# Optimization experiments

Measured on AMD Instinct MI355X. Metric: run time of the kernel, lower is better.

## Reference

```python
import jax, jax.numpy as jnp
import numpy as np
from jax import lax

N = 64          # n (even -> odd=0, add_odd=0)
B = 256         # batch
F = 256         # input_features
ITERS = 10      # sinkhorn iterations


def _conv1d(x, w, b, pad, dil):
    # x: (B, Cin, L), w: (Cout, Cin, K) torch layout
    y = lax.conv_general_dilated(
        x, w, window_strides=(1,), padding=[(pad, pad)],
        rhs_dilation=(dil,), dimension_numbers=("NCH", "OIH", "NCH"))
    return y + b[None, :, None]


def setup_inputs() -> dict:
    key = jax.random.key(0)
    ks = jax.random.split(key, 17)
    s = 0.02
    d = {
        "x": jax.random.normal(ks[0], (B, F), jnp.float32),
        # linear stack (torch Linear layout: (out, in))
        "w1": jax.random.normal(ks[1], (2 * N, F), jnp.float32) * s,
        "b1": jax.random.normal(ks[2], (2 * N,), jnp.float32) * s,
        "w2": jax.random.normal(ks[3], (N * N, 2 * N), jnp.float32) * s,
        "b2": jax.random.normal(ks[4], (N * N,), jnp.float32) * s,
        "w3": jax.random.normal(ks[5], (4 * N * N, N * N), jnp.float32) * s,
        "b3": jax.random.normal(ks[6], (4 * N * N,), jnp.float32) * s,
        # conv stack: 2n->3n->2n->n->n->n, all k=3
        "cw1": jax.random.normal(ks[7], (3 * N, 2 * N, 3), jnp.float32) * s,
        "cb1": jax.random.normal(ks[8], (3 * N,), jnp.float32) * s,
        "cw2": jax.random.normal(ks[9], (2 * N, 3 * N, 3), jnp.float32) * s,
        "cb2": jax.random.normal(ks[10], (2 * N,), jnp.float32) * s,
        "cw3": jax.random.normal(ks[11], (N, 2 * N, 3), jnp.float32) * s,
        "cb3": jax.random.normal(ks[12], (N,), jnp.float32) * s,
        "cw4": jax.random.normal(ks[13], (N, N, 3), jnp.float32) * s,
        "cb4": jax.random.normal(ks[14], (N,), jnp.float32) * s,
        "cw5": jax.random.normal(ks[15], (N, N, 3), jnp.float32) * s,
        "cb5": jax.random.normal(ks[16], (N,), jnp.float32) * s,
    }
    return d


def _sink(x, iters):
    # output = x + 0.001; repeat: row-normalize then col-normalize
    out = x + 0.001

    def body(o, _):
        o = o / jnp.sum(o, axis=2, keepdims=True)  # row_sink: divide each row by its sum
        o = o / jnp.sum(o, axis=1, keepdims=True)  # col_sink: divide each column by its sum
        return o, None

    out, _ = lax.scan(body, out, None, length=iters)
    return out


def reference(x, w1, b1, w2, b2, w3, b3,
              cw1, cb1, cw2, cb2, cw3, cb3, cw4, cb4, cw5, cb5):
    h = x @ w1.T + b1
    h = h @ w2.T + b2
    h = h @ w3.T + b3                      # (B, 4n^2)
    h = h.reshape(B, 2 * N, 2 * N)         # (B, 128, 128)
    # conv1: p=0, d=(n-8)//2=28 (since n>10); rest pad=0, dil=1
    h = _conv1d(h, cw1, cb1, 0, (N - 8) // 2)  # (B, 192, 72)
    h = _conv1d(h, cw2, cb2, 0, 1)             # (B, 128, 70)
    h = _conv1d(h, cw3, cb3, 0, 1)             # (B, 64, 68)
    h = _conv1d(h, cw4, cb4, 0, 1)             # (B, 64, 66)
    h = _conv1d(h, cw5, cb5, 0, 1)             # (B, 64, 64)
    h = h * h                                   # torch.pow(x, 2)
    return _sink(h, ITERS)
```

## Files before the change

kernel.cpp:

```cpp
#include <hip/hip_runtime.h>
#include <hip/hip_bf16.h>

typedef float f32x4 __attribute__((ext_vector_type(4)));
typedef __bf16 bf16x8 __attribute__((ext_vector_type(8)));

typedef __attribute__((address_space(1))) const unsigned int as1_uint;
typedef __attribute__((address_space(3))) unsigned int as3_uint;

__global__ __launch_bounds__(128) void gemm1_k(const float* __restrict__ x,
                                               const float* __restrict__ w1,
                                               const float* __restrict__ b1,
                                               float* __restrict__ h1) {
    __shared__ float xs[256];
    const int m = blockIdx.x, t = threadIdx.x;
    xs[t] = x[m * 256 + t];
    xs[t + 128] = x[m * 256 + 128 + t];
    __syncthreads();
    float acc = b1[t];
    const float4* wr = (const float4*)(w1 + t * 256);
#pragma unroll 8
    for (int k4 = 0; k4 < 64; ++k4) {
        float4 w = wr[k4];
        acc += xs[k4 * 4 + 0] * w.x + xs[k4 * 4 + 1] * w.y +
               xs[k4 * 4 + 2] * w.z + xs[k4 * 4 + 3] * w.w;
    }
    h1[m * 128 + t] = acc;
}

__global__ __launch_bounds__(256) void gemm2_k(const float* __restrict__ h1,
                                               const float* __restrict__ w2,
                                               const float* __restrict__ b2,
                                               char* __restrict__ h2b) {
    __shared__ float As[64][129];
    __shared__ float Bs[64][129];
    const int nb = blockIdx.x, mb = blockIdx.y, t = threadIdx.x;
#pragma unroll
    for (int i = 0; i < 8; ++i) {
        int idx = i * 256 + t;
        int row = idx >> 5, c4 = (idx & 31) * 4;
        float4 a = *(const float4*)(h1 + (mb * 64 + row) * 128 + c4);
        As[row][c4 + 0] = a.x; As[row][c4 + 1] = a.y;
        As[row][c4 + 2] = a.z; As[row][c4 + 3] = a.w;
        float4 bv = *(const float4*)(w2 + (nb * 64 + row) * 128 + c4);
        Bs[row][c4 + 0] = bv.x; Bs[row][c4 + 1] = bv.y;
        Bs[row][c4 + 2] = bv.z; Bs[row][c4 + 3] = bv.w;
    }
    __syncthreads();
    const int tx = t & 15, ty = t >> 4;
    float acc[4][4] = {};
#pragma unroll 4
    for (int k = 0; k < 128; ++k) {
        float a[4], b[4];
#pragma unroll
        for (int i = 0; i < 4; ++i) a[i] = As[ty * 4 + i][k];
#pragma unroll
        for (int j = 0; j < 4; ++j) b[j] = Bs[tx * 4 + j][k];
#pragma unroll
        for (int i = 0; i < 4; ++i)
#pragma unroll
            for (int j = 0; j < 4; ++j) acc[i][j] += a[i] * b[j];
    }
#pragma unroll
    for (int i = 0; i < 4; ++i)
#pragma unroll
        for (int j = 0; j < 4; ++j) {
            int m = mb * 64 + ty * 4 + i;
            int n = nb * 64 + tx * 4 + j;
            float v = acc[i][j] + b2[n];
            int kb = n >> 6, r = n & 63;
            int byte = kb * 32768 + ((m * 128 + (r >> 3) * 16) ^ ((m & 7) << 4)) + (r & 7) * 2;
            *(__bf16*)(h2b + byte) = (__bf16)v;
        }
}

__global__ __launch_bounds__(512, 1) void gemm3_k(const char* __restrict__ Ab,
                                                  const float* __restrict__ W,
                                                  const float* __restrict__ bias,
                                                  float* __restrict__ C) {
    __shared__ __align__(16) char lds[81920];
    const int tid = threadIdx.x;
    const int n0 = blockIdx.x * 64;
    const int lane = tid & 63, wid = tid >> 6;
    const int mrow = tid >> 3, kb8 = tid & 7;

#define ISSUE_A(t, buf)                                                          \
    {                                                                            \
        const char* _s = Ab + (t) * 32768 + wid * 4096 + lane * 16;              \
        char* _d = lds + (buf) * 32768 + wid * 4096;                             \
        __builtin_amdgcn_global_load_lds((as1_uint*)(_s), (as3_uint*)(_d), 16, 0, 0);          \
        __builtin_amdgcn_global_load_lds((as1_uint*)(_s + 1024), (as3_uint*)(_d + 1024), 16, 0, 0); \
        __builtin_amdgcn_global_load_lds((as1_uint*)(_s + 2048), (as3_uint*)(_d + 2048), 16, 0, 0); \
        __builtin_amdgcn_global_load_lds((as1_uint*)(_s + 3072), (as3_uint*)(_d + 3072), 16, 0, 0); \
    }

    float4 w0, w1;
    auto loadW = [&](int t) {
        const float* q = W + (n0 + mrow) * 4096 + t * 64 + kb8 * 8;
        w0 = *(const float4*)q;
        w1 = *(const float4*)(q + 4);
    };
    auto storeW = [&](int buf) {
        bf16x8 p;
        p[0] = (__bf16)w0.x; p[1] = (__bf16)w0.y; p[2] = (__bf16)w0.z; p[3] = (__bf16)w0.w;
        p[4] = (__bf16)w1.x; p[5] = (__bf16)w1.y; p[6] = (__bf16)w1.z; p[7] = (__bf16)w1.w;
        *(bf16x8*)(lds + 65536 + buf * 8192 +
                   ((mrow * 128 + kb8 * 16) ^ ((mrow & 7) << 4))) = p;
    };

    ISSUE_A(0, 0);
    loadW(0);
    __syncthreads();
    storeW(0);
    __syncthreads();

    const int lr = lane & 15, lq = lane >> 4;
    const int wm = wid >> 1, wn = wid & 1;

    f32x4 acc[4][2];
    const f32x4 zero = {0.f, 0.f, 0.f, 0.f};
#pragma unroll
    for (int mi = 0; mi < 4; ++mi)
#pragma unroll
        for (int ni = 0; ni < 2; ++ni) acc[mi][ni] = zero;

    for (int t = 0; t < 64; ++t) {
        const int cur = t & 1;
        if (t < 63) {
            ISSUE_A(t + 1, cur ^ 1);
            loadW(t + 1);
        }
        const char* Ac = lds + cur * 32768;
        const char* Wc = lds + 65536 + cur * 8192;
#pragma unroll
        for (int kk = 0; kk < 2; ++kk) {
            const int kb = kk * 4 + lq;
            bf16x8 af[4], bfv[2];
#pragma unroll
            for (int mi = 0; mi < 4; ++mi) {
                int m = wm * 64 + mi * 16 + lr;
                af[mi] = *(const bf16x8*)(Ac + ((m * 128 + kb * 16) ^ ((m & 7) << 4)));
            }
#pragma unroll
            for (int ni = 0; ni < 2; ++ni) {
                int n = wn * 32 + ni * 16 + lr;
                bfv[ni] = *(const bf16x8*)(Wc + ((n * 128 + kb * 16) ^ ((n & 7) << 4)));
            }
#pragma unroll
            for (int mi = 0; mi < 4; ++mi)
#pragma unroll
                for (int ni = 0; ni < 2; ++ni)
                    acc[mi][ni] = __builtin_amdgcn_mfma_f32_16x16x32_bf16(
                        af[mi], bfv[ni], acc[mi][ni], 0, 0, 0);
        }
        __syncthreads();
        if (t < 63) storeW(cur ^ 1);
        __syncthreads();
    }
#undef ISSUE_A

    float bv[2];
#pragma unroll
    for (int ni = 0; ni < 2; ++ni) bv[ni] = bias[n0 + wn * 32 + ni * 16 + lr];
#pragma unroll
    for (int mi = 0; mi < 4; ++mi)
#pragma unroll
        for (int ni = 0; ni < 2; ++ni) {
            const int n = n0 + wn * 32 + ni * 16 + lr;
#pragma unroll
            for (int r = 0; r < 4; ++r) {
                int m = wm * 64 + mi * 16 + lq * 4 + r;
                C[m * 16384 + n] = acc[mi][ni][r] + bv[ni];
            }
        }
}

template <int CIN, int COUT, int DIL, int MT, int NT>
__device__ __forceinline__ void conv_core(const char* xt, char* wl,
                                          const float* __restrict__ w,
                                          f32x4 (&acc)[MT][NT], int tid) {
    constexpr int RB = CIN * 2;
    const int lane = tid & 63, wid = tid >> 6;
    const int lr = lane & 15, lq = lane >> 4;
    const int cobase = wid * (COUT / 4);
    const f32x4 zero = {0.f, 0.f, 0.f, 0.f};
#pragma unroll
    for (int mi = 0; mi < MT; ++mi)
#pragma unroll
        for (int ni = 0; ni < NT; ++ni) acc[mi][ni] = zero;

    for (int cic = 0; cic < CIN / 32; ++cic) {
        for (int idx = tid; idx < COUT * 4; idx += 256) {
            int co = idx >> 2, cib = idx & 3, ci0 = cic * 32 + cib * 8;
            const float* src = w + co * (CIN * 3) + ci0 * 3;
            float v[24];
#pragma unroll
            for (int u = 0; u < 6; ++u) {
                float4 f = *(const float4*)(src + u * 4);
                v[u * 4 + 0] = f.x; v[u * 4 + 1] = f.y;
                v[u * 4 + 2] = f.z; v[u * 4 + 3] = f.w;
            }
#pragma unroll
            for (int tp = 0; tp < 3; ++tp) {
                bf16x8 pk;
#pragma unroll
                for (int j = 0; j < 8; ++j) pk[j] = (__bf16)v[j * 3 + tp];
                *(bf16x8*)(wl + ((tp * 4 + cib) * COUT + co) * 16) = pk;
            }
        }
        __syncthreads();
#pragma unroll
        for (int tp = 0; tp < 3; ++tp) {
            bf16x8 af[MT];
#pragma unroll
            for (int mi = 0; mi < MT; ++mi)
                af[mi] = *(const bf16x8*)(wl + ((tp * 4 + lq) * COUT + cobase + mi * 16 + lr) * 16);
            bf16x8 bfr[NT];
#pragma unroll
            for (int ni = 0; ni < NT; ++ni) {
                int colX = ni * 16 + lr + tp * DIL;
                bfr[ni] = *(const bf16x8*)(xt + ((colX * RB + (cic * 4 + lq) * 16) ^ ((colX & 7) << 4)));
            }
#pragma unroll
            for (int mi = 0; mi < MT; ++mi)
#pragma unroll
                for (int ni = 0; ni < NT; ++ni)
                    acc[mi][ni] = __builtin_amdgcn_mfma_f32_16x16x32_bf16(
                        af[mi], bfr[ni], acc[mi][ni], 0, 0, 0);
        }
        __syncthreads();
    }
}

template <int COUT, int LOUT, int MT, int NT>
__device__ __forceinline__ void write_xt(char* xt_out, const f32x4 (&acc)[MT][NT],
                                         const float* __restrict__ bias, int tid) {
    constexpr int RBO = COUT * 2;
    const int lane = tid & 63, wid = tid >> 6;
    const int lr = lane & 15, lq = lane >> 4;
    const int cobase = wid * (COUT / 4);
#pragma unroll
    for (int mi = 0; mi < MT; ++mi)
#pragma unroll
        for (int ni = 0; ni < NT; ++ni) {
            int l = ni * 16 + lr;
            if (l < LOUT) {
#pragma unroll
                for (int r = 0; r < 4; ++r) {
                    int co = cobase + mi * 16 + lq * 4 + r;
                    float y = acc[mi][ni][r] + bias[co];
                    int byte = (l * RBO + ((co >> 3) << 4) + (co & 7) * 2) ^ ((l & 7) << 4);
                    *(__bf16*)(xt_out + byte) = (__bf16)y;
                }
            }
        }
}

__global__ __launch_bounds__(256, 1) void convsink_k(
    const float* __restrict__ h3,
    const float* __restrict__ cw1, const float* __restrict__ cb1,
    const float* __restrict__ cw2, const float* __restrict__ cb2,
    const float* __restrict__ cw3, const float* __restrict__ cb3,
    const float* __restrict__ cw4, const float* __restrict__ cb4,
    const float* __restrict__ cw5, const float* __restrict__ cb5,
    float* __restrict__ out) {
    __shared__ __align__(16) char lds[34816 + 31488 + 36864 + 16640];
    char* xtA = lds;
    char* xtB = lds + 34816;
    char* wl = lds + 34816 + 31488;
    float* S = (float*)(lds + 34816 + 31488 + 36864);

    const int b = blockIdx.x, tid = threadIdx.x;
    const float* src = h3 + b * 16384;

#pragma unroll
    for (int i = 0; i < 8; ++i) {
        int idx = i * 256 + tid;
        int l = idx & 127, cib = idx >> 7;
        bf16x8 p;
#pragma unroll
        for (int j = 0; j < 8; ++j) p[j] = (__bf16)src[(cib * 8 + j) * 128 + l];
        *(bf16x8*)(xtA + ((l * 256 + cib * 16) ^ ((l & 7) << 4))) = p;
    }
    __syncthreads();

    {
        f32x4 acc[3][5];
        conv_core<128, 192, 28, 3, 5>(xtA, wl, cw1, acc, tid);
        write_xt<192, 72, 3, 5>(xtB, acc, cb1, tid);
    }
    __syncthreads();
    {
        f32x4 acc[2][5];
        conv_core<192, 128, 1, 2, 5>(xtB, wl, cw2, acc, tid);
        write_xt<128, 70, 2, 5>(xtA, acc, cb2, tid);
    }
    __syncthreads();
    {
        f32x4 acc[1][5];
        conv_core<128, 64, 1, 1, 5>(xtA, wl, cw3, acc, tid);
        write_xt<64, 68, 1, 5>(xtB, acc, cb3, tid);
    }
    __syncthreads();
    {
        f32x4 acc[1][5];
        conv_core<64, 64, 1, 1, 5>(xtB, wl, cw4, acc, tid);
        write_xt<64, 66, 1, 5>(xtA, acc, cb4, tid);
    }
    __syncthreads();
    {
        f32x4 acc[1][4];
        conv_core<64, 64, 1, 1, 4>(xtA, wl, cw5, acc, tid);
        const int lane = tid & 63, wid = tid >> 6;
        const int lr = lane & 15, lq = lane >> 4;
        const int cobase = wid * 16;
#pragma unroll
        for (int ni = 0; ni < 4; ++ni) {
            int l = ni * 16 + lr;
#pragma unroll
            for (int r = 0; r < 4; ++r) {
                int co = cobase + lq * 4 + r;
                float y = acc[0][ni][r] + cb5[co];
                S[co * 65 + l] = y * y + 0.001f;
            }
        }
    }
    __syncthreads();

    const int q = tid & 3, rid = tid >> 2;
    for (int it = 0; it < 10; ++it) {
        float p = 0.f;
#pragma unroll
        for (int j = 0; j < 16; ++j) p += S[rid * 65 + q * 16 + j];
        p += __shfl_xor(p, 1);
        p += __shfl_xor(p, 2);
        float inv = 1.0f / p;
#pragma unroll
        for (int j = 0; j < 16; ++j) S[rid * 65 + q * 16 + j] *= inv;
        __syncthreads();
        float c = 0.f;
#pragma unroll
        for (int i = 0; i < 16; ++i) c += S[(q * 16 + i) * 65 + rid];
        c += __shfl_xor(c, 1);
        c += __shfl_xor(c, 2);
        float invc = 1.0f / c;
#pragma unroll
        for (int i = 0; i < 16; ++i) S[(q * 16 + i) * 65 + rid] *= invc;
        __syncthreads();
    }

#pragma unroll
    for (int i = 0; i < 16; ++i) {
        int idx = i * 256 + tid;
        out[b * 4096 + idx] = S[(idx >> 6) * 65 + (idx & 63)];
    }
}

extern "C" void kernel_launch(void* const* d_in, const int* in_sizes, int n_in,
                              void* d_out, int out_size, void* d_ws, size_t ws_size,
                              hipStream_t stream) {
    const float* x = (const float*)d_in[0];
    const float* w1 = (const float*)d_in[1];
    const float* b1 = (const float*)d_in[2];
    const float* w2 = (const float*)d_in[3];
    const float* b2 = (const float*)d_in[4];
    const float* w3 = (const float*)d_in[5];
    const float* b3 = (const float*)d_in[6];
    const float* cw1 = (const float*)d_in[7];
    const float* cb1 = (const float*)d_in[8];
    const float* cw2 = (const float*)d_in[9];
    const float* cb2 = (const float*)d_in[10];
    const float* cw3 = (const float*)d_in[11];
    const float* cb3 = (const float*)d_in[12];
    const float* cw4 = (const float*)d_in[13];
    const float* cb4 = (const float*)d_in[14];
    const float* cw5 = (const float*)d_in[15];
    const float* cb5 = (const float*)d_in[16];
    float* out = (float*)d_out;

    char* ws = (char*)d_ws;
    float* h1 = (float*)(ws);
    char* h2b = ws + 131072;
    float* h3 = (float*)(ws + 131072 + 2097152);

    gemm1_k<<<256, 128, 0, stream>>>(x, w1, b1, h1);
    gemm2_k<<<dim3(64, 4), 256, 0, stream>>>(h1, w2, b2, h2b);
    gemm3_k<<<256, 512, 0, stream>>>(h2b, w3, b3, h3);
    convsink_k<<<256, 256, 0, stream>>>(h3, cw1, cb1, cw2, cb2, cw3, cb3,
                                        cw4, cb4, cw5, cb5, out);
}
```

Baseline: 150.1 us.

## Triple-buffer A tiles with two-ahead prefetch and a single barrier per step

Extends the A operand staging in the third GEMM from double to triple LDS buffering, with the async global-to-LDS loads issued two iterations ahead. The two full __syncthreads per iteration become a single s_barrier preceded by a manual lgkmcnt wait. Read completion of the A prefetch relies on the in-order vmcnt wait the compiler inserts for the W register loads. The goal is to hide global load latency and cut synchronization stalls, at the cost of more LDS per block (still one block per CU) and fragile hand-managed wait counts.

```diff
diff --git a/kernel.cpp b/kernel.cpp
--- a/kernel.cpp
+++ b/kernel.cpp
@@ -77,41 +77,45 @@
                                                   const float* __restrict__ W,
                                                   const float* __restrict__ bias,
                                                   float* __restrict__ C) {
-    __shared__ __align__(16) char lds[81920];
+    __shared__ __align__(16) char lds[3 * 32768 + 2 * 8192];
+    char* const Wb = lds + 98304;
     const int tid = threadIdx.x;
     const int n0 = blockIdx.x * 64;
     const int lane = tid & 63, wid = tid >> 6;
     const int mrow = tid >> 3, kb8 = tid & 7;
 
-#define ISSUE_A(t, buf)                                                          \
-    {                                                                            \
-        const char* _s = Ab + (t) * 32768 + wid * 4096 + lane * 16;              \
-        char* _d = lds + (buf) * 32768 + wid * 4096;                             \
-        __builtin_amdgcn_global_load_lds((as1_uint*)(_s), (as3_uint*)(_d), 16, 0, 0);          \
+#define ISSUE_A(t, slot)                                                            \
+    {                                                                               \
+        const char* _s = Ab + (t) * 32768 + wid * 4096 + lane * 16;                 \
+        char* _d = lds + (slot) * 32768 + wid * 4096;                               \
+        __builtin_amdgcn_global_load_lds((as1_uint*)(_s), (as3_uint*)(_d), 16, 0, 0);             \
         __builtin_amdgcn_global_load_lds((as1_uint*)(_s + 1024), (as3_uint*)(_d + 1024), 16, 0, 0); \
         __builtin_amdgcn_global_load_lds((as1_uint*)(_s + 2048), (as3_uint*)(_d + 2048), 16, 0, 0); \
         __builtin_amdgcn_global_load_lds((as1_uint*)(_s + 3072), (as3_uint*)(_d + 3072), 16, 0, 0); \
     }
 
-    float4 w0, w1;
+    float4 w0r, w1r;
     auto loadW = [&](int t) {
         const float* q = W + (n0 + mrow) * 4096 + t * 64 + kb8 * 8;
-        w0 = *(const float4*)q;
-        w1 = *(const float4*)(q + 4);
+        w0r = *(const float4*)q;
+        w1r = *(const float4*)(q + 4);
     };
     auto storeW = [&](int buf) {
         bf16x8 p;
-        p[0] = (__bf16)w0.x; p[1] = (__bf16)w0.y; p[2] = (__bf16)w0.z; p[3] = (__bf16)w0.w;
-        p[4] = (__bf16)w1.x; p[5] = (__bf16)w1.y; p[6] = (__bf16)w1.z; p[7] = (__bf16)w1.w;
-        *(bf16x8*)(lds + 65536 + buf * 8192 +
-                   ((mrow * 128 + kb8 * 16) ^ ((mrow & 7) << 4))) = p;
+        p[0] = (__bf16)w0r.x; p[1] = (__bf16)w0r.y; p[2] = (__bf16)w0r.z; p[3] = (__bf16)w0r.w;
+        p[4] = (__bf16)w1r.x; p[5] = (__bf16)w1r.y; p[6] = (__bf16)w1r.z; p[7] = (__bf16)w1r.w;
+        *(bf16x8*)(Wb + buf * 8192 + ((mrow * 128 + kb8 * 16) ^ ((mrow & 7) << 4))) = p;
     };
 
+    loadW(0);
     ISSUE_A(0, 0);
-    loadW(0);
-    __syncthreads();
+    ISSUE_A(1, 1);
     storeW(0);
-    __syncthreads();
+    asm volatile("s_waitcnt vmcnt(4)" ::: "memory");
+    __builtin_amdgcn_sched_barrier(0);
+    asm volatile("s_waitcnt lgkmcnt(0)" ::: "memory");
+    __builtin_amdgcn_sched_barrier(0);
+    __builtin_amdgcn_s_barrier();
 
     const int lr = lane & 15, lq = lane >> 4;
     const int wm = wid >> 1, wn = wid & 1;
@@ -123,14 +127,15 @@
 #pragma unroll
         for (int ni = 0; ni < 2; ++ni) acc[mi][ni] = zero;
 
+    int sA = 0;
+    int sA2 = 2;
     for (int t = 0; t < 64; ++t) {
         const int cur = t & 1;
-        if (t < 63) {
-            ISSUE_A(t + 1, cur ^ 1);
-            loadW(t + 1);
-        }
-        const char* Ac = lds + cur * 32768;
-        const char* Wc = lds + 65536 + cur * 8192;
+        if (t < 63) loadW(t + 1);
+        if (t < 62) ISSUE_A(t + 2, sA2);
+
+        const char* Ac = lds + sA * 32768;
+        const char* Wc = Wb + cur * 8192;
 #pragma unroll
         for (int kk = 0; kk < 2; ++kk) {
             const int kb = kk * 4 + lq;
@@ -152,9 +157,15 @@
                     acc[mi][ni] = __builtin_amdgcn_mfma_f32_16x16x32_bf16(
                         af[mi], bfv[ni], acc[mi][ni], 0, 0, 0);
         }
-        __syncthreads();
-        if (t < 63) storeW(cur ^ 1);
-        __syncthreads();
+
+        if (t < 63) {
+            storeW(cur ^ 1);
+            asm volatile("s_waitcnt lgkmcnt(0)" ::: "memory");
+            __builtin_amdgcn_sched_barrier(0);
+            __builtin_amdgcn_s_barrier();
+        }
+        sA = (sA == 2) ? 0 : sA + 1;
+        sA2 = (sA2 == 2) ? 0 : sA2 + 1;
     }
 #undef ISSUE_A
 
```

After: 144.2 us. 1.04x faster.

## Drop LDS staging in gemm3 and load MFMA fragments directly from global

Applied to the files above, without the earlier changes.

Rewrites gemm3 so each wave loads its A (bf16) and W (fp32, converted in registers) MFMA fragments straight from global memory into registers, double-buffered across k-steps, with no LDS and no block barriers. gemm2 now writes h2 in an unswizzled layout to match. This removes the LDS round trip and the syncthreads pairs per iteration. In exchange, A and W fragments are reloaded redundantly by several waves, so L2/global traffic rises, and register pressure goes up. The final loop iteration also issues a redundant load of tile 62.

```diff
diff --git a/kernel.cpp b/kernel.cpp
--- a/kernel.cpp
+++ b/kernel.cpp
@@ -3,9 +3,6 @@
 
 typedef float f32x4 __attribute__((ext_vector_type(4)));
 typedef __bf16 bf16x8 __attribute__((ext_vector_type(8)));
-
-typedef __attribute__((address_space(1))) const unsigned int as1_uint;
-typedef __attribute__((address_space(3))) unsigned int as3_uint;
 
 __global__ __launch_bounds__(128) void gemm1_k(const float* __restrict__ x,
                                                const float* __restrict__ w1,
@@ -68,54 +65,63 @@
             int n = nb * 64 + tx * 4 + j;
             float v = acc[i][j] + b2[n];
             int kb = n >> 6, r = n & 63;
-            int byte = kb * 32768 + ((m * 128 + (r >> 3) * 16) ^ ((m & 7) << 4)) + (r & 7) * 2;
+            int byte = kb * 32768 + m * 128 + (r >> 3) * 16 + (r & 7) * 2;
             *(__bf16*)(h2b + byte) = (__bf16)v;
         }
 }
 
-__global__ __launch_bounds__(512, 1) void gemm3_k(const char* __restrict__ Ab,
-                                                  const float* __restrict__ W,
-                                                  const float* __restrict__ bias,
-                                                  float* __restrict__ C) {
-    __shared__ __align__(16) char lds[81920];
+__device__ __forceinline__ bf16x8 pack8(const float4& lo, const float4& hi) {
+    bf16x8 p;
+    p[0] = (__bf16)lo.x; p[1] = (__bf16)lo.y; p[2] = (__bf16)lo.z; p[3] = (__bf16)lo.w;
+    p[4] = (__bf16)hi.x; p[5] = (__bf16)hi.y; p[6] = (__bf16)hi.z; p[7] = (__bf16)hi.w;
+    return p;
+}
+
+__global__ __launch_bounds__(512) void gemm3_k(const char* __restrict__ Ab,
+                                               const float* __restrict__ W,
+                                               const float* __restrict__ bias,
+                                               float* __restrict__ C) {
     const int tid = threadIdx.x;
     const int n0 = blockIdx.x * 64;
     const int lane = tid & 63, wid = tid >> 6;
-    const int mrow = tid >> 3, kb8 = tid & 7;
-
-#define ISSUE_A(t, buf)                                                          \
-    {                                                                            \
-        const char* _s = Ab + (t) * 32768 + wid * 4096 + lane * 16;              \
-        char* _d = lds + (buf) * 32768 + wid * 4096;                             \
-        __builtin_amdgcn_global_load_lds((as1_uint*)(_s), (as3_uint*)(_d), 16, 0, 0);          \
-        __builtin_amdgcn_global_load_lds((as1_uint*)(_s + 1024), (as3_uint*)(_d + 1024), 16, 0, 0); \
-        __builtin_amdgcn_global_load_lds((as1_uint*)(_s + 2048), (as3_uint*)(_d + 2048), 16, 0, 0); \
-        __builtin_amdgcn_global_load_lds((as1_uint*)(_s + 3072), (as3_uint*)(_d + 3072), 16, 0, 0); \
-    }
-
-    float4 w0, w1;
-    auto loadW = [&](int t) {
-        const float* q = W + (n0 + mrow) * 4096 + t * 64 + kb8 * 8;
-        w0 = *(const float4*)q;
-        w1 = *(const float4*)(q + 4);
-    };
-    auto storeW = [&](int buf) {
-        bf16x8 p;
-        p[0] = (__bf16)w0.x; p[1] = (__bf16)w0.y; p[2] = (__bf16)w0.z; p[3] = (__bf16)w0.w;
-        p[4] = (__bf16)w1.x; p[5] = (__bf16)w1.y; p[6] = (__bf16)w1.z; p[7] = (__bf16)w1.w;
-        *(bf16x8*)(lds + 65536 + buf * 8192 +
-                   ((mrow * 128 + kb8 * 16) ^ ((mrow & 7) << 4))) = p;
-    };
-
-    ISSUE_A(0, 0);
-    loadW(0);
-    __syncthreads();
-    storeW(0);
-    __syncthreads();
-
     const int lr = lane & 15, lq = lane >> 4;
     const int wm = wid >> 1, wn = wid & 1;
 
+    const char* Abase = Ab + (wm * 64 + lr) * 128 + lq * 16;
+    const float* Wp = W + (size_t)(n0 + wn * 32 + lr) * 4096 + lq * 8;
+
+#define LOADA(dst, t)                                                   \
+    {                                                                   \
+        const char* _p = Abase + (t) * 32768;                           \
+        _Pragma("unroll") for (int mi = 0; mi < 4; ++mi) {              \
+            dst[mi][0] = *(const bf16x8*)(_p + mi * 2048);              \
+            dst[mi][1] = *(const bf16x8*)(_p + mi * 2048 + 64);         \
+        }                                                               \
+    }
+#define LOADW(d0, d1, t)                                                \
+    {                                                                   \
+        _Pragma("unroll") for (int ni = 0; ni < 2; ++ni) {              \
+            const float* _q = Wp + ni * (16 * 4096) + (t) * 64;         \
+            d0[ni][0] = *(const float4*)_q;                             \
+            d1[ni][0] = *(const float4*)(_q + 4);                       \
+            d0[ni][1] = *(const float4*)(_q + 32);                      \
+            d1[ni][1] = *(const float4*)(_q + 36);                      \
+        }                                                               \
+    }
+#define STEP(aR, w0R, w1R)                                                       \
+    {                                                                            \
+        _Pragma("unroll") for (int kk = 0; kk < 2; ++kk) {                       \
+            bf16x8 bf0 = pack8(w0R[0][kk], w1R[0][kk]);                          \
+            bf16x8 bf1 = pack8(w0R[1][kk], w1R[1][kk]);                          \
+            _Pragma("unroll") for (int mi = 0; mi < 4; ++mi) {                   \
+                acc[mi][0] = __builtin_amdgcn_mfma_f32_16x16x32_bf16(            \
+                    aR[mi][kk], bf0, acc[mi][0], 0, 0, 0);                       \
+                acc[mi][1] = __builtin_amdgcn_mfma_f32_16x16x32_bf16(            \
+                    aR[mi][kk], bf1, acc[mi][1], 0, 0, 0);                       \
+            }                                                                    \
+        }                                                                        \
+    }
+
     f32x4 acc[4][2];
     const f32x4 zero = {0.f, 0.f, 0.f, 0.f};
 #pragma unroll
@@ -123,40 +129,24 @@
 #pragma unroll
         for (int ni = 0; ni < 2; ++ni) acc[mi][ni] = zero;
 
-    for (int t = 0; t < 64; ++t) {
-        const int cur = t & 1;
-        if (t < 63) {
-            ISSUE_A(t + 1, cur ^ 1);
-            loadW(t + 1);
-        }
-        const char* Ac = lds + cur * 32768;
-        const char* Wc = lds + 65536 + cur * 8192;
-#pragma unroll
-        for (int kk = 0; kk < 2; ++kk) {
-            const int kb = kk * 4 + lq;
-            bf16x8 af[4], bfv[2];
-#pragma unroll
-            for (int mi = 0; mi < 4; ++mi) {
-                int m = wm * 64 + mi * 16 + lr;
-                af[mi] = *(const bf16x8*)(Ac + ((m * 128 + kb * 16) ^ ((m & 7) << 4)));
-            }
-#pragma unroll
-            for (int ni = 0; ni < 2; ++ni) {
-                int n = wn * 32 + ni * 16 + lr;
-                bfv[ni] = *(const bf16x8*)(Wc + ((n * 128 + kb * 16) ^ ((n & 7) << 4)));
-            }
-#pragma unroll
-            for (int mi = 0; mi < 4; ++mi)
-#pragma unroll
-                for (int ni = 0; ni < 2; ++ni)
-                    acc[mi][ni] = __builtin_amdgcn_mfma_f32_16x16x32_bf16(
-                        af[mi], bfv[ni], acc[mi][ni], 0, 0, 0);
-        }
-        __syncthreads();
-        if (t < 63) storeW(cur ^ 1);
-        __syncthreads();
-    }
-#undef ISSUE_A
+    bf16x8 a0[4][2], a1[4][2];
+    float4 wA0[2][2], wB0[2][2], wA1[2][2], wB1[2][2];
+
+    LOADA(a0, 0);
+    LOADW(wA0, wB0, 0);
+#pragma unroll 1
+    for (int t = 0; t < 64; t += 2) {
+        LOADA(a1, t + 1);
+        LOADW(wA1, wB1, t + 1);
+        STEP(a0, wA0, wB0);
+        const int t2 = (t + 2 < 64) ? t + 2 : 62;
+        LOADA(a0, t2);
+        LOADW(wA0, wB0, t2);
+        STEP(a1, wA1, wB1);
+    }
+#undef LOADA
+#undef LOADW
+#undef STEP
 
     float bv[2];
 #pragma unroll
```

New measurement: 314.6 us. 2.1x slower.

## Split-K gemm3 into two halves with bf16 partials summed in convsink

Applied to the files above, without the earlier changes.

The third GEMM now splits its K dimension across two blocks per column tile, doubling the grid from 256 to 512 workgroups so more CUs are busy. Each half writes a bf16 partial result, and the conv/sinkhorn kernel adds the two partials plus the bias while loading its input. This removes the fp32 h3 write in favour of two bf16 partial buffers, so intermediate traffic stays about the same while K-loop latency per block is halved. The cost is an extra rounding step, since partials are stored in bf16 before summation, and an extra global read in the conv prologue.

```diff
diff --git a/kernel.cpp b/kernel.cpp
--- a/kernel.cpp
+++ b/kernel.cpp
@@ -75,40 +75,42 @@
 
 __global__ __launch_bounds__(512, 1) void gemm3_k(const char* __restrict__ Ab,
                                                   const float* __restrict__ W,
-                                                  const float* __restrict__ bias,
-                                                  float* __restrict__ C) {
+                                                  char* __restrict__ parts) {
     __shared__ __align__(16) char lds[81920];
     const int tid = threadIdx.x;
-    const int n0 = blockIdx.x * 64;
+    const int nb = blockIdx.x >> 1, ks = blockIdx.x & 1;
+    const int n0 = nb * 64;
     const int lane = tid & 63, wid = tid >> 6;
     const int mrow = tid >> 3, kb8 = tid & 7;
 
-#define ISSUE_A(t, buf)                                                          \
-    {                                                                            \
-        const char* _s = Ab + (t) * 32768 + wid * 4096 + lane * 16;              \
-        char* _d = lds + (buf) * 32768 + wid * 4096;                             \
-        __builtin_amdgcn_global_load_lds((as1_uint*)(_s), (as3_uint*)(_d), 16, 0, 0);          \
+#define ISSUE_A(kt, buf)                                                            \
+    {                                                                               \
+        const char* _s = Ab + (kt) * 32768 + wid * 4096 + lane * 16;                \
+        char* _d = lds + (buf) * 32768 + wid * 4096;                                \
+        __builtin_amdgcn_global_load_lds((as1_uint*)(_s), (as3_uint*)(_d), 16, 0, 0);             \
         __builtin_amdgcn_global_load_lds((as1_uint*)(_s + 1024), (as3_uint*)(_d + 1024), 16, 0, 0); \
         __builtin_amdgcn_global_load_lds((as1_uint*)(_s + 2048), (as3_uint*)(_d + 2048), 16, 0, 0); \
         __builtin_amdgcn_global_load_lds((as1_uint*)(_s + 3072), (as3_uint*)(_d + 3072), 16, 0, 0); \
     }
 
-    float4 w0, w1;
-    auto loadW = [&](int t) {
-        const float* q = W + (n0 + mrow) * 4096 + t * 64 + kb8 * 8;
-        w0 = *(const float4*)q;
-        w1 = *(const float4*)(q + 4);
+    float4 w0r, w1r;
+    auto loadW = [&](int kt) {
+        const float* q = W + (n0 + mrow) * 4096 + kt * 64 + kb8 * 8;
+        w0r = *(const float4*)q;
+        w1r = *(const float4*)(q + 4);
     };
     auto storeW = [&](int buf) {
         bf16x8 p;
-        p[0] = (__bf16)w0.x; p[1] = (__bf16)w0.y; p[2] = (__bf16)w0.z; p[3] = (__bf16)w0.w;
-        p[4] = (__bf16)w1.x; p[5] = (__bf16)w1.y; p[6] = (__bf16)w1.z; p[7] = (__bf16)w1.w;
+        p[0] = (__bf16)w0r.x; p[1] = (__bf16)w0r.y; p[2] = (__bf16)w0r.z; p[3] = (__bf16)w0r.w;
+        p[4] = (__bf16)w1r.x; p[5] = (__bf16)w1r.y; p[6] = (__bf16)w1r.z; p[7] = (__bf16)w1r.w;
         *(bf16x8*)(lds + 65536 + buf * 8192 +
                    ((mrow * 128 + kb8 * 16) ^ ((mrow & 7) << 4))) = p;
     };
 
-    ISSUE_A(0, 0);
-    loadW(0);
+    const int kt0 = ks * 32;
+
+    ISSUE_A(kt0, 0);
+    loadW(kt0);
     __syncthreads();
     storeW(0);
     __syncthreads();
@@ -123,11 +125,11 @@
 #pragma unroll
         for (int ni = 0; ni < 2; ++ni) acc[mi][ni] = zero;
 
-    for (int t = 0; t < 64; ++t) {
+    for (int t = 0; t < 32; ++t) {
         const int cur = t & 1;
-        if (t < 63) {
-            ISSUE_A(t + 1, cur ^ 1);
-            loadW(t + 1);
+        if (t < 31) {
+            ISSUE_A(kt0 + t + 1, cur ^ 1);
+            loadW(kt0 + t + 1);
         }
         const char* Ac = lds + cur * 32768;
         const char* Wc = lds + 65536 + cur * 8192;
@@ -153,14 +155,12 @@
                         af[mi], bfv[ni], acc[mi][ni], 0, 0, 0);
         }
         __syncthreads();
-        if (t < 63) storeW(cur ^ 1);
+        if (t < 31) storeW(cur ^ 1);
         __syncthreads();
     }
 #undef ISSUE_A
 
-    float bv[2];
-#pragma unroll
-    for (int ni = 0; ni < 2; ++ni) bv[ni] = bias[n0 + wn * 32 + ni * 16 + lr];
+    __bf16* P = (__bf16*)(parts + ks * 8388608);
 #pragma unroll
     for (int mi = 0; mi < 4; ++mi)
 #pragma unroll
@@ -169,7 +169,7 @@
 #pragma unroll
             for (int r = 0; r < 4; ++r) {
                 int m = wm * 64 + mi * 16 + lq * 4 + r;
-                C[m * 16384 + n] = acc[mi][ni][r] + bv[ni];
+                P[m * 16384 + n] = (__bf16)acc[mi][ni][r];
             }
         }
 }
@@ -256,7 +256,7 @@
 }
 
 __global__ __launch_bounds__(256, 1) void convsink_k(
-    const float* __restrict__ h3,
+    const char* __restrict__ parts, const float* __restrict__ b3,
     const float* __restrict__ cw1, const float* __restrict__ cb1,
     const float* __restrict__ cw2, const float* __restrict__ cb2,
     const float* __restrict__ cw3, const float* __restrict__ cb3,
@@ -270,7 +270,8 @@
     float* S = (float*)(lds + 34816 + 31488 + 36864);
 
     const int b = blockIdx.x, tid = threadIdx.x;
-    const float* src = h3 + b * 16384;
+    const __bf16* p0 = (const __bf16*)parts + (size_t)b * 16384;
+    const __bf16* p1 = (const __bf16*)(parts + 8388608) + (size_t)b * 16384;
 
 #pragma unroll
     for (int i = 0; i < 8; ++i) {
@@ -278,7 +279,11 @@
         int l = idx & 127, cib = idx >> 7;
         bf16x8 p;
 #pragma unroll
-        for (int j = 0; j < 8; ++j) p[j] = (__bf16)src[(cib * 8 + j) * 128 + l];
+        for (int j = 0; j < 8; ++j) {
+            int n = (cib * 8 + j) * 128 + l;
+            float v = (float)p0[n] + (float)p1[n] + b3[n];
+            p[j] = (__bf16)v;
+        }
         *(bf16x8*)(xtA + ((l * 256 + cib * 16) ^ ((l & 7) << 4))) = p;
     }
     __syncthreads();
@@ -380,11 +385,11 @@
     char* ws = (char*)d_ws;
     float* h1 = (float*)(ws);
     char* h2b = ws + 131072;
-    float* h3 = (float*)(ws + 131072 + 2097152);
+    char* parts = ws + 131072 + 2097152;
 
     gemm1_k<<<256, 128, 0, stream>>>(x, w1, b1, h1);
     gemm2_k<<<dim3(64, 4), 256, 0, stream>>>(h1, w2, b2, h2b);
-    gemm3_k<<<256, 512, 0, stream>>>(h2b, w3, b3, h3);
-    convsink_k<<<256, 256, 0, stream>>>(h3, cw1, cb1, cw2, cb2, cw3, cb3,
-                                        cw4, cb4, cw5, cb5, out);
-}
+    gemm3_k<<<512, 512, 0, stream>>>(h2b, w3, parts);
+    convsink_k<<<256, 256, 0, stream>>>(parts, b3, cw1, cb1, cw2, cb2,
+                                        cw3, cb3, cw4, cb4, cw5, cb5, out);
+}
```

After: 131.2 us. 12.6% less time.
